# Performance work log

Hardware: AMD Instinct MI355X
Metric: run time of the kernel (lower is better)

Reference implementation:

```python
import jax, jax.numpy as jnp
import numpy as np

S = 2048
NODE_DIM = 128
H = 8          # num_heads
C = 32         # num_channels


def setup_inputs() -> dict:
    key = jax.random.key(0)
    ks = jax.random.split(key, 12)
    inv = lambda n: 1.0 / np.sqrt(n)
    inp = {
        "nodes": jax.random.normal(ks[0], (S, NODE_DIM), dtype=jnp.float32),
        "pos": jax.random.uniform(ks[1], (S, 3), dtype=jnp.float32),
        "rot": jax.random.normal(ks[2], (S, 4), dtype=jnp.float32),
        # eqx.nn.Linear weights are (out_features, in_features)
        "w_nodes_kq": jax.random.uniform(ks[3], (H * C * 2, NODE_DIM), minval=-inv(NODE_DIM), maxval=inv(NODE_DIM)),
        "b_nodes_kq": jax.random.uniform(ks[4], (H * C * 2,), minval=-inv(NODE_DIM), maxval=inv(NODE_DIM)),
        "w_pos_kq": jax.random.uniform(ks[5], (H * C * 2, 6), minval=-inv(6), maxval=inv(6)),
        "b_pos_kq": jax.random.uniform(ks[6], (H * C * 2,), minval=-inv(6), maxval=inv(6)),
        "w_rot_kq": jax.random.uniform(ks[7], (H * C * 2, 4), minval=-inv(4), maxval=inv(4)),  # no bias
        "w_values": jax.random.uniform(ks[8], (NODE_DIM * H * 3, NODE_DIM), minval=-inv(NODE_DIM), maxval=inv(NODE_DIM)),
        "b_values": jax.random.uniform(ks[9], (NODE_DIM * H * 3,), minval=-inv(NODE_DIM), maxval=inv(NODE_DIM)),
    }
    return inp


def reference(nodes, pos, rot, w_nodes_kq, b_nodes_kq, w_pos_kq, b_pos_kq,
              w_rot_kq, w_values, b_values):
    seq_len = nodes.shape[0]
    # circular positional features: [S, 6]
    pos_feat = jnp.concatenate([jnp.cos(2 * jnp.pi * pos), jnp.sin(2 * jnp.pi * pos)], axis=-1)

    # values: [S, 3H, node_dim]
    val = (nodes @ w_values.T + b_values).reshape(seq_len, 3 * H, -1)

    # per-source k/q projections, each -> [S, H, C]
    nodes_k, nodes_q = jnp.split((nodes @ w_nodes_kq.T + b_nodes_kq).reshape(seq_len, H, -1), 2, -1)
    pos_k, pos_q = jnp.split((pos_feat @ w_pos_kq.T + b_pos_kq).reshape(seq_len, H, -1), 2, -1)
    rot_k, rot_q = jnp.split((rot @ w_rot_kq.T).reshape(seq_len, H, -1), 2, -1)

    # concat over head axis -> [S, 3H, C]
    k = jnp.concatenate([nodes_k, pos_k, rot_k], axis=-2)
    q = jnp.concatenate([nodes_q, pos_q, rot_q], axis=-2)

    # logits: [S, S, 3H]; square the last H (rotation) heads' sub-logits
    logits = jnp.einsum('ihc,jhc->ijh', k, q)
    logits = logits.at[..., -H:].set(jnp.square(logits[..., -H:]))

    # softmax over j (axis=-2), then weighted sum of values over j and heads
    att = jax.nn.softmax(logits, axis=-2)
    out = jnp.einsum('ijh,jhd->id', att, val)  # [S, node_dim]
    return out
```

## Files before the change

kernel.cpp:

```cpp
#include <hip/hip_runtime.h>
#include <hip/hip_bf16.h>
#include <math.h>

#define SEQ 2048
#define NHEAD 24
#define CDIM 32
#define VDIM 128

typedef short bf16x8 __attribute__((ext_vector_type(8)));
typedef float f32x4 __attribute__((ext_vector_type(4)));

#define L2E 1.44269504088896f
#define SQRT_L2E 1.20112240878645f

#if __has_builtin(__builtin_amdgcn_exp2f)
#define EXP2(x) __builtin_amdgcn_exp2f(x)
#else
#define EXP2(x) exp2f(x)
#endif

__device__ unsigned short g_kkp[(size_t)24 * 128 * 2 * 64 * 8];
__device__ unsigned short g_qv[(size_t)24 * 32 * 24 * 64 * 8];
__device__ unsigned short g_wp[(size_t)224 * 4 * 2 * 64 * 8];
__device__ unsigned short g_np[(size_t)128 * 4 * 2 * 64 * 8];

__device__ __forceinline__ unsigned short f2b(float x) {
  union { float f; unsigned u; } v; v.f = x;
  unsigned r = v.u + 0x7FFF + ((v.u >> 16) & 1);
  return (unsigned short)(r >> 16);
}
__device__ __forceinline__ float b2f(unsigned short u) {
  union { unsigned u32; float f; } x; x.u32 = ((unsigned)u) << 16; return x.f;
}
__device__ __forceinline__ unsigned pk2(float a, float b) {
  __hip_bfloat162 t = __float22bfloat162_rn(float2{a, b});
  union { __hip_bfloat162 h; unsigned u; } c; c.h = t; return c.u;
}
__device__ __forceinline__ unsigned long long pack64(const float* p) {
  return ((unsigned long long)pk2(p[2], p[3]) << 32) | pk2(p[0], p[1]);
}
__device__ __forceinline__ void gld16(const unsigned short* g, unsigned short* l) {
  __builtin_amdgcn_global_load_lds(
      (const __attribute__((address_space(1))) unsigned int*)g,
      (__attribute__((address_space(3))) unsigned int*)l, 16, 0, 0);
}

__global__ __launch_bounds__(256) void k_prep(const float* __restrict__ nodes,
                                              const float* __restrict__ w_v,
                                              const float* __restrict__ w_n) {
  const int tid = blockIdx.x * 256 + threadIdx.x;
  const int fg = tid >> 6, lane = tid & 63;
  const int e0 = (lane >> 4) * 8;
  const float* p;
  unsigned short* dst;
  if (blockIdx.x < 224) {
    const int colblk = fg >> 2, ks = fg & 3;
    const int ocol = colblk * 16 + (lane & 15);
    const float* src = (ocol < 3072) ? (w_v + (size_t)ocol * 128)
                                     : (w_n + (size_t)(ocol - 3072) * 128);
    p = src + ks * 32 + e0;
    dst = g_wp + (size_t)fg * 1024;
  } else {
    const int fg2 = fg - 224 * 4;
    const int rowblk = fg2 >> 2, ks = fg2 & 3;
    p = nodes + (size_t)(rowblk * 16 + (lane & 15)) * 128 + ks * 32 + e0;
    dst = g_np + (size_t)fg2 * 1024;
  }
  float4 f0 = *(const float4*)p;
  float4 f1 = *(const float4*)(p + 4);
  float ff[8] = {f0.x, f0.y, f0.z, f0.w, f1.x, f1.y, f1.z, f1.w};
  bf16x8 hi, lo;
#pragma unroll
  for (int e = 0; e < 8; ++e) {
    unsigned short h2 = f2b(ff[e]);
    hi[e] = (short)h2;
    lo[e] = (short)f2b(ff[e] - b2f(h2));
  }
  *(bf16x8*)(dst + (size_t)lane * 8) = hi;
  *(bf16x8*)(dst + 512 + (size_t)lane * 8) = lo;
}

__global__ __launch_bounds__(256) void k_proj(const float* __restrict__ b_v,
                                              const float* __restrict__ b_n) {
  const int jt = blockIdx.x;
  const int bo = blockIdx.y;
  const bool is_kq = bo >= 48;
  const float* bsrc = is_kq ? b_n : b_v;
  const int o0b = is_kq ? (bo - 48) * 64 : bo * 64;
  const int tx = threadIdx.x;
  const int w = tx >> 6, lane = tx & 63;
  const int m = lane & 15, quad = lane >> 4;

  __shared__ __align__(16) unsigned short bst[32][64][8];
  __shared__ __align__(16) float res[4][64][20];

  const unsigned short* wp = g_wp + ((size_t)bo * 32 + w * 8) * 512 + (size_t)lane * 8;
#pragma unroll
  for (int s = 0; s < 8; ++s)
    gld16(wp + s * 512, &bst[w * 8 + s][0][0]);

  bf16x8 ah[4], al[4];
  const unsigned short* np = g_np + (size_t)(jt * 4 + w) * 4096 + (size_t)lane * 8;
#pragma unroll
  for (int ks = 0; ks < 4; ++ks) {
    ah[ks] = *(const bf16x8*)(np + ks * 1024);
    al[ks] = *(const bf16x8*)(np + ks * 1024 + 512);
  }
  __syncthreads();

  f32x4 C[4];
#pragma unroll
  for (int ob = 0; ob < 4; ++ob) {
    f32x4 acc = {0.f, 0.f, 0.f, 0.f};
#pragma unroll
    for (int ks = 0; ks < 4; ++ks) {
      bf16x8 bh = *(const bf16x8*)&bst[ob * 8 + ks * 2][lane][0];
      bf16x8 bl = *(const bf16x8*)&bst[ob * 8 + ks * 2 + 1][lane][0];
      acc = __builtin_amdgcn_mfma_f32_16x16x32_bf16(ah[ks], bh, acc, 0, 0, 0);
      acc = __builtin_amdgcn_mfma_f32_16x16x32_bf16(al[ks], bh, acc, 0, 0, 0);
      acc = __builtin_amdgcn_mfma_f32_16x16x32_bf16(ah[ks], bl, acc, 0, 0, 0);
    }
    C[ob] = acc;
  }
#pragma unroll
  for (int ob = 0; ob < 4; ++ob) {
    float bias = bsrc[o0b + ob * 16 + m];
#pragma unroll
    for (int r = 0; r < 4; ++r)
      res[w][ob * 16 + m][quad * 4 + r] = C[ob][r] + bias;
  }
  if (!is_kq) {
    const int g = bo >> 1, dbb = (bo & 1) * 4;
    const int jc = w >> 1, khb = (w & 1) * 2;
    const int rowq = quad;
#pragma unroll
    for (int oct = 0; oct < 2; ++oct) {
      f32x4 v0 = *(const f32x4*)&res[w][rowq * 16 + m][oct * 8];
      f32x4 v1 = *(const f32x4*)&res[w][rowq * 16 + m][oct * 8 + 4];
      bf16x8 pk;
#pragma unroll
      for (int e = 0; e < 4; ++e) {
        pk[e]     = (short)f2b(v0[e]);
        pk[4 + e] = (short)f2b(v1[e]);
      }
      ((bf16x8*)g_qv)[(((size_t)g * 32 + jt) * 24 + 8 + jc * 8 + dbb + rowq) * 64
                      + (khb + oct) * 16 + m] = pk;
    }
  } else {
    const int h = bo - 48;
    const int rowq = quad;
    {
      bf16x8 hi, lo;
#pragma unroll
      for (int e = 0; e < 8; ++e) {
        float v = res[w][rowq * 8 + e][m] * L2E;
        unsigned short h2 = f2b(v);
        hi[e] = (short)h2;
        lo[e] = (short)f2b(v - b2f(h2));
      }
      size_t base = ((size_t)(h * 128 + jt * 4 + w) * 2) * 512 + (size_t)(rowq * 16 + m) * 8;
      *(bf16x8*)(g_kkp + base) = hi;
      *(bf16x8*)(g_kkp + base + 512) = lo;
    }
    {
      bf16x8 hi, lo;
#pragma unroll
      for (int e = 0; e < 8; ++e) {
        float v = res[w][32 + rowq * 8 + e][m];
        unsigned short h2 = f2b(v);
        hi[e] = (short)h2;
        lo[e] = (short)f2b(v - b2f(h2));
      }
      size_t base = (((size_t)h * 32 + jt) * 24 + w * 2) * 512 + (size_t)(rowq * 16 + m) * 8;
      *(bf16x8*)(g_qv + base) = hi;
      *(bf16x8*)(g_qv + base + 512) = lo;
    }
  }
}

__device__ __forceinline__ void repack_store(const unsigned* __restrict__ res,
                                             int oh, int it16, int tx, int head_base) {
#pragma unroll
  for (int t2 = 0; t2 < 2; ++t2) {
    int cid = tx + t2 * 256;
    int hl  = cid >> 7;
    int kq  = (cid >> 6) & 1;
    int row = cid & 63;
    int m = row & 15, kb = row >> 4;
    int ob = hl * 64 + kq * 32 + kb * 8;
    bf16x8 hi, lo;
#pragma unroll
    for (int e = 0; e < 8; ++e) {
      unsigned pk = res[(ob + e) * 17 + m];
      hi[e] = (short)(pk >> 16);
      lo[e] = (short)(pk & 0xffff);
    }
    int gh = head_base + oh * 4 + hl;
    if (kq == 0) {
      size_t base = ((size_t)(gh * 128 + it16) * 2) * 512 + (size_t)row * 8;
      *(bf16x8*)(g_kkp + base) = hi;
      *(bf16x8*)(g_kkp + base + 512) = lo;
    } else {
      int jt = it16 >> 2, jb = it16 & 3;
      size_t base = (((size_t)gh * 32 + jt) * 24 + jb * 2) * 512 + (size_t)row * 8;
      *(bf16x8*)(g_qv + base) = hi;
      *(bf16x8*)(g_qv + base + 512) = lo;
    }
  }
}

__global__ __launch_bounds__(256) void k_posrot(const float* __restrict__ pos,
                                                const float* __restrict__ rot,
                                                const float* __restrict__ w_p,
                                                const float* __restrict__ b_p,
                                                const float* __restrict__ w_r) {
  const int it16 = blockIdx.x;
  const int oh   = blockIdx.y;
  const int br   = blockIdx.z;
  const int tx = threadIdx.x;
  const int i0 = it16 * 16;

  __shared__ float pf_sh[16][8];
  __shared__ float rr_sh[16][4];
  __shared__ unsigned res[256 * 17];

  if (br == 0) {
    if (tx < 48) {
      int r = tx / 3, t = tx - r * 3;
      float p = pos[(i0 + r) * 3 + t];
      pf_sh[r][t]     = cosf(6.283185307179586f * p);
      pf_sh[r][t + 3] = sinf(6.283185307179586f * p);
    }
  } else {
    if (tx < 64) {
      int r = tx >> 2, t = tx & 3;
      rr_sh[r][t] = rot[(i0 + r) * 4 + t];
    }
  }
  __syncthreads();

  const int og = tx & 63, ig = tx >> 6;

  if (br == 0) {
#pragma unroll
    for (int oo = 0; oo < 4; ++oo) {
      int o = oh * 256 + oo * 64 + og;
      float bb = b_p[o];
      float w0 = w_p[o * 6 + 0], w1 = w_p[o * 6 + 1], w2 = w_p[o * 6 + 2];
      float w3 = w_p[o * 6 + 3], w4 = w_p[o * 6 + 4], w5 = w_p[o * 6 + 5];
      float sc = ((o & 63) < 32) ? L2E : 1.f;
#pragma unroll
      for (int ii = 0; ii < 4; ++ii) {
        int i = ig * 4 + ii;
        float v = bb + pf_sh[i][0] * w0 + pf_sh[i][1] * w1 + pf_sh[i][2] * w2
                     + pf_sh[i][3] * w3 + pf_sh[i][4] * w4 + pf_sh[i][5] * w5;
        v *= sc;
        unsigned short hi = f2b(v);
        unsigned short lo = f2b(v - b2f(hi));
        res[(oo * 64 + og) * 17 + i] = ((unsigned)hi << 16) | lo;
      }
    }
  } else {
#pragma unroll
    for (int oo = 0; oo < 4; ++oo) {
      int o = oh * 256 + oo * 64 + og;
      float w0 = w_r[o * 4 + 0], w1 = w_r[o * 4 + 1], w2 = w_r[o * 4 + 2], w3 = w_r[o * 4 + 3];
      float sc = ((o & 63) < 32) ? SQRT_L2E : 1.f;
#pragma unroll
      for (int ii = 0; ii < 4; ++ii) {
        int i = ig * 4 + ii;
        float v = (rr_sh[i][0] * w0 + rr_sh[i][1] * w1 + rr_sh[i][2] * w2 + rr_sh[i][3] * w3) * sc;
        unsigned short hi = f2b(v);
        unsigned short lo = f2b(v - b2f(hi));
        res[(oo * 64 + og) * 17 + i] = ((unsigned)hi << 16) | lo;
      }
    }
  }
  __syncthreads();
  repack_store(res, oh, it16, tx, 8 + br * 8);
}

__global__ __launch_bounds__(256) void k_zero(float* __restrict__ out) {
  out[blockIdx.x * 256 + threadIdx.x] = 0.f;
}

__global__ __launch_bounds__(256) void k_attn(float* __restrict__ out) {
  const int it = blockIdx.x;
  const int g  = blockIdx.y;
  const int tx = threadIdx.x;
  const int w = tx >> 6, lane = tx & 63;
  const int quad = lane >> 4, n = lane & 15;
  const int iblk = it * 4 + w;

  __shared__ __align__(16) unsigned short stage[2][24][64][8];
  __shared__ __align__(16) unsigned long long p_lds[4][64][2];
  __shared__ __align__(16) float bc[4][16];

  const bf16x8* kp = (const bf16x8*)g_kkp + (size_t)(g * 128 + iblk) * 2 * 64;
  const bf16x8 khi = kp[lane], klo = kp[64 + lane];

  f32x4 oacc[8];
#pragma unroll
  for (int db = 0; db < 8; ++db)
#pragma unroll
    for (int r = 0; r < 4; ++r) oacc[db][r] = 0.f;

  float m_run = -3.0e38f, l_run = 0.f;
  const bool is_rot = (g >= 16);
  const int pin = (lane & 56) | ((lane ^ (lane >> 3)) & 7);
  const int wrow0 = (quad >> 1) * 16 + n;
  const int wrow1 = wrow0 + 32;
  const int pr0 = (wrow0 & 56) | ((wrow0 ^ (wrow0 >> 3)) & 7);
  const int pr1 = (wrow1 & 56) | ((wrow1 ^ (wrow1 >> 3)) & 7);
  const int whalf = quad & 1;

  const unsigned short* qv = g_qv + ((size_t)g * 32 * 24 + w * 6) * 512 + (size_t)lane * 8;

#define STG(nb)                                          \
  { gld16(qv,             &stage[nb][w * 6 + 0][0][0]);  \
    gld16(qv + 512,       &stage[nb][w * 6 + 1][0][0]);  \
    gld16(qv + 1024,      &stage[nb][w * 6 + 2][0][0]);  \
    gld16(qv + 1536,      &stage[nb][w * 6 + 3][0][0]);  \
    gld16(qv + 2048,      &stage[nb][w * 6 + 4][0][0]);  \
    gld16(qv + 2560,      &stage[nb][w * 6 + 5][0][0]); }

  STG(0)

  for (int jt = 0; jt < 32; ++jt) {
    const int buf = jt & 1;
    __syncthreads();
    qv += 24 * 512;
    if (jt < 31) STG(buf ^ 1)

    const bf16x8* st = (const bf16x8*)&stage[buf][0][0][0];
    f32x4 S[4];
#pragma unroll
    for (int jb = 0; jb < 4; ++jb) {
      bf16x8 qh = st[(jb * 2) * 64 + lane], ql = st[(jb * 2 + 1) * 64 + lane];
      f32x4 a = {0.f, 0.f, 0.f, 0.f};
      a = __builtin_amdgcn_mfma_f32_16x16x32_bf16(qh, khi, a, 0, 0, 0);
      a = __builtin_amdgcn_mfma_f32_16x16x32_bf16(ql, khi, a, 0, 0, 0);
      a = __builtin_amdgcn_mfma_f32_16x16x32_bf16(qh, klo, a, 0, 0, 0);
      S[jb] = a;
    }
    if (is_rot) {
#pragma unroll
      for (int jb = 0; jb < 4; ++jb)
#pragma unroll
        for (int r = 0; r < 4; ++r) S[jb][r] *= S[jb][r];
    }
    float mb = S[0][0];
#pragma unroll
    for (int jb = 0; jb < 4; ++jb)
#pragma unroll
      for (int r = 0; r < 4; ++r) mb = fmaxf(mb, S[jb][r]);
    mb = fmaxf(mb, __shfl_xor(mb, 16));
    mb = fmaxf(mb, __shfl_xor(mb, 32));
    if (__ballot(mb > m_run)) {
      float m_new = fmaxf(m_run, mb);
      float alpha = EXP2(m_run - m_new);
      l_run *= alpha;
      m_run = m_new;
      if (lane < 16) bc[w][lane] = alpha;
      f32x4 av = *(const f32x4*)&bc[w][quad * 4];
#pragma unroll
      for (int db = 0; db < 8; ++db) {
        oacc[db][0] *= av[0]; oacc[db][1] *= av[1];
        oacc[db][2] *= av[2]; oacc[db][3] *= av[3];
      }
    }
    float p[4][4];
    float s = 0.f;
#pragma unroll
    for (int jb = 0; jb < 4; ++jb)
#pragma unroll
      for (int r = 0; r < 4; ++r) {
        p[jb][r] = EXP2(S[jb][r] - m_run);
        s += p[jb][r];
      }
    s += __shfl_xor(s, 16);
    s += __shfl_xor(s, 32);
    l_run += s;
    p_lds[w][pr0][whalf] = pack64(p[0]);
    p_lds[w][pr1][whalf] = pack64(p[1]);
    bf16x8 a0 = *(const bf16x8*)&p_lds[w][pin][0];
#pragma unroll
    for (int db = 0; db < 8; ++db)
      oacc[db] = __builtin_amdgcn_mfma_f32_16x16x32_bf16(a0, st[(8 + db) * 64 + lane], oacc[db], 0, 0, 0);
    p_lds[w][pr0][whalf] = pack64(p[2]);
    p_lds[w][pr1][whalf] = pack64(p[3]);
    bf16x8 a1 = *(const bf16x8*)&p_lds[w][pin][0];
#pragma unroll
    for (int db = 0; db < 8; ++db)
      oacc[db] = __builtin_amdgcn_mfma_f32_16x16x32_bf16(a1, st[(16 + db) * 64 + lane], oacc[db], 0, 0, 0);
  }
  float linv = 1.f / l_run;
  if (lane < 16) bc[w][lane] = linv;
  f32x4 lv = *(const f32x4*)&bc[w][quad * 4];
  const int ibase = it * 64 + w * 16 + quad * 4;
#pragma unroll
  for (int db = 0; db < 8; ++db)
#pragma unroll
    for (int r = 0; r < 4; ++r)
      atomicAdd(&out[(size_t)(ibase + r) * VDIM + db * 16 + n], oacc[db][r] * lv[r]);
}

extern "C" void kernel_launch(void* const* d_in, const int* in_sizes, int n_in,
                              void* d_out, int out_size, void* d_ws, size_t ws_size,
                              hipStream_t stream) {
  const float* nodes = (const float*)d_in[0];
  const float* pos   = (const float*)d_in[1];
  const float* rot   = (const float*)d_in[2];
  const float* w_n   = (const float*)d_in[3];
  const float* b_n   = (const float*)d_in[4];
  const float* w_p   = (const float*)d_in[5];
  const float* b_p   = (const float*)d_in[6];
  const float* w_r   = (const float*)d_in[7];
  const float* w_v   = (const float*)d_in[8];
  const float* b_v   = (const float*)d_in[9];
  float* out = (float*)d_out;

  k_zero<<<dim3((SEQ * VDIM) / 256), 256, 0, stream>>>(out);
  k_prep<<<dim3(352), 256, 0, stream>>>(nodes, w_v, w_n);
  k_posrot<<<dim3(128, 2, 2), 256, 0, stream>>>(pos, rot, w_p, b_p, w_r);
  k_proj<<<dim3(32, 56), 256, 0, stream>>>(b_v, b_n);
  k_attn<<<dim3(32, NHEAD), 256, 0, stream>>>(out);
}
```

Measured before the change: 174.7 us.

## Software-pipeline PV MFMAs across iterations and defer row-sum reductions

The P·V MFMAs for tile jt are deferred to the start of iteration jt+1. The V fragments are held in 16 registers (vprev), so the value MFMAs overlap the next tile's QK and softmax math. The per-tile cross-lane row-sum shuffles are replaced by a per-lane partial sum that is reduced once at the end. The max shuffles now only run when the ballot fires. LDS broadcasts of alpha and 1/l are replaced by ds_bpermute, and launch bounds request 3 blocks per SM. The extra held registers (16 bf16x8) raise register pressure, which the occupancy hint may force into spills.

Measured after the change: 168.1 us. 3.8% less time.

```diff
diff --git a/kernel.cpp b/kernel.cpp
--- a/kernel.cpp
+++ b/kernel.cpp
@@ -38,6 +38,11 @@
 }
 __device__ __forceinline__ unsigned long long pack64(const float* p) {
   return ((unsigned long long)pk2(p[2], p[3]) << 32) | pk2(p[0], p[1]);
+}
+__device__ __forceinline__ float bperm_f(int srclane, float v) {
+  union { float f; int i; } u; u.f = v;
+  u.i = __builtin_amdgcn_ds_bpermute(srclane * 4, u.i);
+  return u.f;
 }
 __device__ __forceinline__ void gld16(const unsigned short* g, unsigned short* l) {
   __builtin_amdgcn_global_load_lds(
@@ -284,7 +289,7 @@
   out[blockIdx.x * 256 + threadIdx.x] = 0.f;
 }
 
-__global__ __launch_bounds__(256) void k_attn(float* __restrict__ out) {
+__global__ __launch_bounds__(256, 3) void k_attn(float* __restrict__ out) {
   const int it = blockIdx.x;
   const int g  = blockIdx.y;
   const int tx = threadIdx.x;
@@ -294,7 +299,6 @@
 
   __shared__ __align__(16) unsigned short stage[2][24][64][8];
   __shared__ __align__(16) unsigned long long p_lds[4][64][2];
-  __shared__ __align__(16) float bc[4][16];
 
   const bf16x8* kp = (const bf16x8*)g_kkp + (size_t)(g * 128 + iblk) * 2 * 64;
   const bf16x8 khi = kp[lane], klo = kp[64 + lane];
@@ -305,7 +309,7 @@
 #pragma unroll
     for (int r = 0; r < 4; ++r) oacc[db][r] = 0.f;
 
-  float m_run = -3.0e38f, l_run = 0.f;
+  float m_run = -3.0e38f, l_part = 0.f;
   const bool is_rot = (g >= 16);
   const int pin = (lane & 56) | ((lane ^ (lane >> 3)) & 7);
   const int wrow0 = (quad >> 1) * 16 + n;
@@ -326,9 +330,22 @@
 
   STG(0)
 
+  bf16x8 a0 = {}, a1 = {};
+  bf16x8 vprev[16];
+
   for (int jt = 0; jt < 32; ++jt) {
     const int buf = jt & 1;
     __syncthreads();
+
+    if (jt) {
+#pragma unroll
+      for (int db = 0; db < 8; ++db)
+        oacc[db] = __builtin_amdgcn_mfma_f32_16x16x32_bf16(a0, vprev[db], oacc[db], 0, 0, 0);
+#pragma unroll
+      for (int db = 0; db < 8; ++db)
+        oacc[db] = __builtin_amdgcn_mfma_f32_16x16x32_bf16(a1, vprev[8 + db], oacc[db], 0, 0, 0);
+    }
+
     qv += 24 * 512;
     if (jt < 31) STG(buf ^ 1)
 
@@ -349,20 +366,21 @@
 #pragma unroll
         for (int r = 0; r < 4; ++r) S[jb][r] *= S[jb][r];
     }
-    float mb = S[0][0];
+    float mloc = S[0][0];
 #pragma unroll
     for (int jb = 0; jb < 4; ++jb)
 #pragma unroll
-      for (int r = 0; r < 4; ++r) mb = fmaxf(mb, S[jb][r]);
-    mb = fmaxf(mb, __shfl_xor(mb, 16));
-    mb = fmaxf(mb, __shfl_xor(mb, 32));
-    if (__ballot(mb > m_run)) {
+      for (int r = 0; r < 4; ++r) mloc = fmaxf(mloc, S[jb][r]);
+    if (__ballot(mloc > m_run)) {
+      float mb = fmaxf(mloc, __shfl_xor(mloc, 16));
+      mb = fmaxf(mb, __shfl_xor(mb, 32));
       float m_new = fmaxf(m_run, mb);
       float alpha = EXP2(m_run - m_new);
-      l_run *= alpha;
       m_run = m_new;
-      if (lane < 16) bc[w][lane] = alpha;
-      f32x4 av = *(const f32x4*)&bc[w][quad * 4];
+      l_part *= alpha;
+      f32x4 av;
+#pragma unroll
+      for (int r = 0; r < 4; ++r) av[r] = bperm_f(quad * 4 + r, alpha);
 #pragma unroll
       for (int db = 0; db < 8; ++db) {
         oacc[db][0] *= av[0]; oacc[db][1] *= av[1];
@@ -370,33 +388,36 @@
       }
     }
     float p[4][4];
-    float s = 0.f;
 #pragma unroll
     for (int jb = 0; jb < 4; ++jb)
 #pragma unroll
       for (int r = 0; r < 4; ++r) {
         p[jb][r] = EXP2(S[jb][r] - m_run);
-        s += p[jb][r];
-      }
-    s += __shfl_xor(s, 16);
-    s += __shfl_xor(s, 32);
-    l_run += s;
+        l_part += p[jb][r];
+      }
     p_lds[w][pr0][whalf] = pack64(p[0]);
     p_lds[w][pr1][whalf] = pack64(p[1]);
-    bf16x8 a0 = *(const bf16x8*)&p_lds[w][pin][0];
-#pragma unroll
-    for (int db = 0; db < 8; ++db)
-      oacc[db] = __builtin_amdgcn_mfma_f32_16x16x32_bf16(a0, st[(8 + db) * 64 + lane], oacc[db], 0, 0, 0);
+    a0 = *(const bf16x8*)&p_lds[w][pin][0];
     p_lds[w][pr0][whalf] = pack64(p[2]);
     p_lds[w][pr1][whalf] = pack64(p[3]);
-    bf16x8 a1 = *(const bf16x8*)&p_lds[w][pin][0];
-#pragma unroll
-    for (int db = 0; db < 8; ++db)
-      oacc[db] = __builtin_amdgcn_mfma_f32_16x16x32_bf16(a1, st[(16 + db) * 64 + lane], oacc[db], 0, 0, 0);
-  }
-  float linv = 1.f / l_run;
-  if (lane < 16) bc[w][lane] = linv;
-  f32x4 lv = *(const f32x4*)&bc[w][quad * 4];
+    a1 = *(const bf16x8*)&p_lds[w][pin][0];
+#pragma unroll
+    for (int f = 0; f < 16; ++f) vprev[f] = st[(8 + f) * 64 + lane];
+  }
+#pragma unroll
+  for (int db = 0; db < 8; ++db)
+    oacc[db] = __builtin_amdgcn_mfma_f32_16x16x32_bf16(a0, vprev[db], oacc[db], 0, 0, 0);
+#pragma unroll
+  for (int db = 0; db < 8; ++db)
+    oacc[db] = __builtin_amdgcn_mfma_f32_16x16x32_bf16(a1, vprev[8 + db], oacc[db], 0, 0, 0);
+
+  float l = l_part;
+  l += __shfl_xor(l, 16);
+  l += __shfl_xor(l, 32);
+  float linv = 1.f / l;
+  f32x4 lv;
+#pragma unroll
+  for (int r = 0; r < 4; ++r) lv[r] = bperm_f(quad * 4 + r, linv);
   const int ibase = it * 64 + w * 16 + quad * 4;
 #pragma unroll
   for (int db = 0; db < 8; ++db)
```
